# Optimization experiments

Hardware: AMD Instinct MI355X
Metric: run time of the kernel (lower is better)

## Reference

```python
import jax, jax.numpy as jnp
import numpy as np

N = 100000      # nodes
E = 1000000     # edges
D_IN = 64       # in_channels
HID = 64        # hid_channels
ENC = 64        # encoding_dim
OUT = 2         # out_channels (classes)
EDGE_DIM = 32   # TimeEncode dim == edge_dim
HEADS = 2
HD = HID // 2   # per-head channels (32)


def _p(k, shape):
    s = 1.0 / np.sqrt(shape[0])
    return jax.random.uniform(k, shape, jnp.float32, -s, s)


def setup_inputs() -> dict:
    key = jax.random.key(0)
    ks = jax.random.split(key, 40)
    inp = {
        "x": jax.random.normal(ks[0], (N, D_IN), jnp.float32),
        "edge_index": jax.random.randint(ks[1], (2, E), 0, N),
        "node_time": jax.random.uniform(ks[2], (N,), jnp.float32) * 100.0,
        "edge_time": jax.random.uniform(ks[3], (E, 1), jnp.float32) * 100.0,
        "node_mean_out_time_interval": jax.random.uniform(ks[4], (N,), jnp.float32) * 10.0,
        "node_out_degree": jax.random.uniform(ks[5], (N,), jnp.float32) * 50.0,
        "y": jax.random.randint(ks[6], (N,), 0, OUT),
        "train_mask": jnp.ones((N,), bool),
        # TimeEncode: cos(t W + b)
        "time_w": _p(ks[7], (1, EDGE_DIM)), "time_b": jnp.zeros((EDGE_DIM,), jnp.float32),
        # TemporalFrequencyEncoder / DegreeEncoder: Linear(1, ENC)
        "tf_w": _p(ks[8], (1, ENC)), "tf_b": jnp.zeros((ENC,), jnp.float32),
        "deg_w": _p(ks[9], (1, ENC)), "deg_b": jnp.zeros((ENC,), jnp.float32),
        # lin: Linear(in, hid)
        "lin_w": _p(ks[10], (D_IN, HID)), "lin_b": jnp.zeros((HID,), jnp.float32),
        # TransformerConv projections (heads*HD = HID)
        "Wq": _p(ks[11], (HID, HEADS * HD)), "bq": jnp.zeros((HEADS * HD,), jnp.float32),
        "Wk": _p(ks[12], (HID, HEADS * HD)), "bk": jnp.zeros((HEADS * HD,), jnp.float32),
        "Wv": _p(ks[13], (HID, HEADS * HD)), "bv": jnp.zeros((HEADS * HD,), jnp.float32),
        "We": _p(ks[14], (EDGE_DIM, HEADS * HD)), "be": jnp.zeros((HEADS * HD,), jnp.float32),
        "Wskip": _p(ks[15], (HID, HEADS * HD)), "bskip": jnp.zeros((HEADS * HD,), jnp.float32),
        # size-2 context attention
        "wenc_w": _p(ks[16], (ENC, ENC)), "wenc_b": jnp.zeros((ENC,), jnp.float32),
        "wx_w": _p(ks[17], (HID, ENC)), "wx_b": jnp.zeros((ENC,), jnp.float32),
        # lin_combine: Linear(hid+enc, hid)
        "comb_w": _p(ks[18], (HID + ENC, HID)), "comb_b": jnp.zeros((HID,), jnp.float32),
        # out: Linear(hid, out)
        "out_w": _p(ks[19], (HID, OUT)), "out_b": jnp.zeros((OUT,), jnp.float32),
    }
    return inp


def reference(x, edge_index, node_time, edge_time, node_mean_out_time_interval,
              node_out_degree, y, train_mask,
              time_w, time_b, tf_w, tf_b, deg_w, deg_b, lin_w, lin_b,
              Wq, bq, Wk, bk, Wv, bv, We, be, Wskip, bskip,
              wenc_w, wenc_b, wx_w, wx_b, comb_w, comb_b, out_w, out_b):
    src, dst = edge_index[0], edge_index[1]

    # relative edge time -> TimeEncode (cos features), used as edge_attr [E, 32]
    rel_t = node_time[src][:, None] - edge_time          # [E,1]
    rel_t_enc = jnp.cos(rel_t @ time_w + time_b)         # [E,EDGE_DIM]

    h = jax.nn.relu(x @ lin_w + lin_b)                   # [N,HID] (dropout = identity, eval)

    # TransformerConv (PyG math): per-edge attention + scatter-softmax aggregate
    q = (h @ Wq + bq).reshape(N, HEADS, HD)[dst]          # [E,H,HD]
    e = (rel_t_enc @ We + be).reshape(E, HEADS, HD)       # [E,H,HD]
    k = (h @ Wk + bk).reshape(N, HEADS, HD)[src] + e
    v = (h @ Wv + bv).reshape(N, HEADS, HD)[src] + e
    alpha = (q * k).sum(-1) / np.float32(np.sqrt(HD))     # [E,H]
    m = jax.ops.segment_max(alpha, dst, num_segments=N)   # stable softmax per dst node
    ea = jnp.exp(alpha - m[dst])
    denom = jax.ops.segment_sum(ea, dst, num_segments=N)
    a = ea / (denom[dst] + 1e-16)
    agg = jax.ops.segment_sum(a[:, :, None] * v, dst, num_segments=N)
    h1 = agg.reshape(N, HEADS * HD) + h @ Wskip + bskip   # concat heads + root skip

    # size-2 context attention over (temporal-frequency, degree) encodings
    tf_enc = node_mean_out_time_interval[:, None] @ tf_w + tf_b   # [N,ENC]
    deg_enc = node_out_degree[:, None] @ deg_w + deg_b            # [N,ENC]
    enc = jnp.stack((tf_enc, deg_enc), axis=1)                    # [N,2,ENC]
    enc_proj = jnp.tanh(enc @ wenc_w + wenc_b)                    # [N,2,ENC]
    x_proj = jnp.tanh(h1 @ wx_w + wx_b)                           # [N,ENC]
    score = jax.nn.softmax(jnp.einsum('nkd,nd->nk', enc_proj, x_proj), axis=1)  # [N,2]
    context = enc[:, 0] * score[:, 0:1] + enc[:, 1] * score[:, 1:2]

    h1 = jnp.concatenate((h1, context), axis=1) @ comb_w + comb_b  # [N,HID]
    logp = jax.nn.log_softmax(h1 @ out_w + out_b, axis=1)          # [N,OUT]
    return (h1, logp, y, train_mask)
```

## Files before the change

kernel.cpp:

```cpp
#include <hip/hip_runtime.h>
#include <hip/hip_fp16.h>

#define DEV __device__ __forceinline__

typedef _Float16 f16x8 __attribute__((ext_vector_type(8)));
typedef float f32x4 __attribute__((ext_vector_type(4)));

DEV float mask_val(const unsigned char* mb, int n) {
  unsigned b0 = mb[0], b1 = mb[1], b2 = mb[2], b3 = mb[3];
  if (b0 <= 1u && b1 == b0 && b2 == b0 && b3 == b0) {
    return mb[n] ? 1.f : 0.f;
  } else if (b1 == 0u && b2 == 0u && b3 == 0u) {
    return ((const int*)mb)[n] ? 1.f : 0.f;
  } else {
    return (((const float*)mb)[n] != 0.f) ? 1.f : 0.f;
  }
}

DEV float head_sum32(float x) {
  x += __int_as_float(__builtin_amdgcn_ds_swizzle(__float_as_int(x), 0x041F));
  x += __int_as_float(__builtin_amdgcn_ds_swizzle(__float_as_int(x), 0x081F));
  x += __int_as_float(__builtin_amdgcn_ds_swizzle(__float_as_int(x), 0x101F));
  x += __int_as_float(__builtin_amdgcn_ds_swizzle(__float_as_int(x), 0x201F));
  x += __int_as_float(__builtin_amdgcn_ds_swizzle(__float_as_int(x), 0x401F));
  return x;
}

__global__ void k_precompute(const float* __restrict__ tf_w, const float* __restrict__ tf_b,
                             const float* __restrict__ deg_w, const float* __restrict__ deg_b,
                             const float* __restrict__ wenc_w, const float* __restrict__ wenc_b,
                             const float* __restrict__ comb_w, float* __restrict__ cbuf) {
  int c = threadIdx.x;
  float A0 = 0, B0 = 0, A1 = 0, B1 = 0, P0 = 0, Q0 = 0, P1 = 0, Q1 = 0;
  for (int j = 0; j < 64; ++j) {
    float w  = wenc_w[j * 64 + c];
    float cw = comb_w[(64 + j) * 64 + c];
    float twj = tf_w[j], tbj = tf_b[j], dwj = deg_w[j], dbj = deg_b[j];
    A0 += twj * w;  B0 += tbj * w;
    A1 += dwj * w;  B1 += dbj * w;
    P0 += twj * cw; Q0 += tbj * cw;
    P1 += dwj * cw; Q1 += dbj * cw;
  }
  float wb = wenc_b[c];
  cbuf[c]       = A0; cbuf[64 + c]  = B0 + wb;
  cbuf[128 + c] = A1; cbuf[192 + c] = B1 + wb;
  cbuf[256 + c] = P0; cbuf[320 + c] = Q0;
  cbuf[384 + c] = P1; cbuf[448 + c] = Q1;
}

__global__ __launch_bounds__(256) void k_wcvt(
    const float* __restrict__ lin_w, const float* __restrict__ Wq,
    const float* __restrict__ Wk, const float* __restrict__ Wv,
    const float* __restrict__ Wsk, _Float16* __restrict__ wt) {
  const float* Ws[5] = {lin_w, Wq, Wk, Wv, Wsk};
  int idx = blockIdx.x * 256 + threadIdx.x;
  if (idx < 5 * 4096) {
    int s = idx >> 12, r = idx & 4095;
    int j = r >> 6, c = r & 63;
    wt[(s << 12) + c * 64 + j] = (_Float16)Ws[s][j * 64 + c];
  }
}

__global__ __launch_bounds__(256) void k_node_proj(
    const float* __restrict__ x, const _Float16* __restrict__ wt,
    const float* __restrict__ lin_b, const float* __restrict__ bq,
    const float* __restrict__ bk, const float* __restrict__ bv,
    const float* __restrict__ bsk, const float* __restrict__ be,
    float* __restrict__ q, __half2* __restrict__ kvp,
    float* __restrict__ skipout, int N) {
  __shared__ _Float16 H[4][16 * 72];
  const int tid = threadIdx.x;
  const int lane = tid & 63;
  const int wv = tid >> 6;
  const int mrow = lane & 15;
  const int kgrp = lane >> 4;
  const float invs = 0.17677669529663687f;
  float b_lin[4], b_q[4], b_k[4], b_v[4], b_sk[4];
#pragma unroll
  for (int nt = 0; nt < 4; ++nt) {
    const int cc = nt * 16 + mrow;
    b_lin[nt] = lin_b[cc];
    b_q[nt] = bq[cc];
    b_k[nt] = bk[cc] + be[cc];
    b_v[nt] = bv[cc] + be[cc];
    b_sk[nt] = bsk[cc];
  }
  _Float16* Hw = H[wv];
  const int ntiles = (N + 63) >> 6;
  for (int tile = blockIdx.x; tile < ntiles; tile += gridDim.x) {
    const int base = tile << 6;
    const int rowA = base + wv * 16 + mrow;
    const int rclamp = (rowA < N) ? rowA : (N - 1);
    const float* xr = x + (size_t)rclamp * 64 + kgrp * 8;
    const float4 u0 = *(const float4*)xr;
    const float4 u1 = *(const float4*)(xr + 4);
    const float4 u2 = *(const float4*)(xr + 32);
    const float4 u3 = *(const float4*)(xr + 36);
    const f16x8 a0 = {(_Float16)u0.x, (_Float16)u0.y, (_Float16)u0.z, (_Float16)u0.w,
                      (_Float16)u1.x, (_Float16)u1.y, (_Float16)u1.z, (_Float16)u1.w};
    const f16x8 a1 = {(_Float16)u2.x, (_Float16)u2.y, (_Float16)u2.z, (_Float16)u2.w,
                      (_Float16)u3.x, (_Float16)u3.y, (_Float16)u3.z, (_Float16)u3.w};
#pragma unroll
    for (int nt = 0; nt < 4; ++nt) {
      const _Float16* wb0 = wt + (nt * 16 + mrow) * 64 + kgrp * 8;
      const f16x8 B0 = *(const f16x8*)wb0;
      const f16x8 B1 = *(const f16x8*)(wb0 + 32);
      f32x4 C = {0.f, 0.f, 0.f, 0.f};
      C = __builtin_amdgcn_mfma_f32_16x16x32_f16(a0, B0, C, 0, 0, 0);
      C = __builtin_amdgcn_mfma_f32_16x16x32_f16(a1, B1, C, 0, 0, 0);
#pragma unroll
      for (int r = 0; r < 4; ++r) {
        const float hval = fmaxf(C[r] + b_lin[nt], 0.f);
        Hw[(kgrp * 4 + r) * 72 + nt * 16 + mrow] = (_Float16)hval;
      }
    }
    const f16x8 ha0 = *(const f16x8*)(Hw + mrow * 72 + kgrp * 8);
    const f16x8 ha1 = *(const f16x8*)(Hw + mrow * 72 + 32 + kgrp * 8);
    const int orow0 = base + wv * 16 + kgrp * 4;
#pragma unroll
    for (int nt = 0; nt < 4; ++nt) {
      const _Float16* wb0 = wt + 4096 + (nt * 16 + mrow) * 64 + kgrp * 8;
      const f16x8 B0 = *(const f16x8*)wb0;
      const f16x8 B1 = *(const f16x8*)(wb0 + 32);
      f32x4 C = {0.f, 0.f, 0.f, 0.f};
      C = __builtin_amdgcn_mfma_f32_16x16x32_f16(ha0, B0, C, 0, 0, 0);
      C = __builtin_amdgcn_mfma_f32_16x16x32_f16(ha1, B1, C, 0, 0, 0);
#pragma unroll
      for (int r = 0; r < 4; ++r) {
        const int orow = orow0 + r;
        if (orow < N) q[(size_t)orow * 64 + nt * 16 + mrow] = (C[r] + b_q[nt]) * invs;
      }
    }
#pragma unroll
    for (int nt = 0; nt < 4; ++nt) {
      const _Float16* wk0 = wt + 2 * 4096 + (nt * 16 + mrow) * 64 + kgrp * 8;
      const _Float16* wv0 = wt + 3 * 4096 + (nt * 16 + mrow) * 64 + kgrp * 8;
      const f16x8 Bk0 = *(const f16x8*)wk0;
      const f16x8 Bk1 = *(const f16x8*)(wk0 + 32);
      const f16x8 Bv0 = *(const f16x8*)wv0;
      const f16x8 Bv1 = *(const f16x8*)(wv0 + 32);
      f32x4 Ck = {0.f, 0.f, 0.f, 0.f};
      f32x4 Cv = {0.f, 0.f, 0.f, 0.f};
      Ck = __builtin_amdgcn_mfma_f32_16x16x32_f16(ha0, Bk0, Ck, 0, 0, 0);
      Ck = __builtin_amdgcn_mfma_f32_16x16x32_f16(ha1, Bk1, Ck, 0, 0, 0);
      Cv = __builtin_amdgcn_mfma_f32_16x16x32_f16(ha0, Bv0, Cv, 0, 0, 0);
      Cv = __builtin_amdgcn_mfma_f32_16x16x32_f16(ha1, Bv1, Cv, 0, 0, 0);
#pragma unroll
      for (int r = 0; r < 4; ++r) {
        const int orow = orow0 + r;
        if (orow < N)
          kvp[(size_t)orow * 64 + nt * 16 + mrow] =
              __halves2half2(__float2half_rn(Ck[r] + b_k[nt]), __float2half_rn(Cv[r] + b_v[nt]));
      }
    }
#pragma unroll
    for (int nt = 0; nt < 4; ++nt) {
      const _Float16* wb0 = wt + 4 * 4096 + (nt * 16 + mrow) * 64 + kgrp * 8;
      const f16x8 B0 = *(const f16x8*)wb0;
      const f16x8 B1 = *(const f16x8*)(wb0 + 32);
      f32x4 C = {0.f, 0.f, 0.f, 0.f};
      C = __builtin_amdgcn_mfma_f32_16x16x32_f16(ha0, B0, C, 0, 0, 0);
      C = __builtin_amdgcn_mfma_f32_16x16x32_f16(ha1, B1, C, 0, 0, 0);
#pragma unroll
      for (int r = 0; r < 4; ++r) {
        const int orow = orow0 + r;
        if (orow < N) skipout[(size_t)orow * 64 + nt * 16 + mrow] = C[r] + b_sk[nt];
      }
    }
  }
}

__global__ __launch_bounds__(256) void k_hist(const int* __restrict__ ei, int* __restrict__ counts, int E) {
  int i = blockIdx.x * 256 + threadIdx.x;
  if (i < E) atomicAdd(&counts[ei[E + i]], 1);
}

__global__ __launch_bounds__(256) void k_scan1(const int* __restrict__ counts, int* __restrict__ excl,
                                               int* __restrict__ bsum, int N) {
  __shared__ int s[256];
  const int t = threadIdx.x;
  const int idx = blockIdx.x * 256 + t;
  int val = (idx < N) ? counts[idx] : 0;
  s[t] = val;
  __syncthreads();
  for (int d = 1; d < 256; d <<= 1) {
    int add = (t >= d) ? s[t - d] : 0;
    __syncthreads();
    s[t] += add;
    __syncthreads();
  }
  if (idx < N) excl[idx] = s[t] - val;
  if (t == 255) bsum[blockIdx.x] = s[255];
}

__global__ __launch_bounds__(1024) void k_scan2(int* __restrict__ bsum, int B) {
  __shared__ int sm[1024];
  const int t = threadIdx.x;
  if (B <= 1024) {
    int val = (t < B) ? bsum[t] : 0;
    sm[t] = val;
    __syncthreads();
    for (int d = 1; d < 1024; d <<= 1) {
      int add = (t >= d) ? sm[t - d] : 0;
      __syncthreads();
      sm[t] += add;
      __syncthreads();
    }
    if (t < B) bsum[t] = sm[t] - val;
  } else if (t == 0) {
    int acc = 0;
    for (int i = 0; i < B; ++i) { int tt = bsum[i]; bsum[i] = acc; acc += tt; }
  }
}

__global__ __launch_bounds__(256) void k_scan3(const int* __restrict__ bsum, int* __restrict__ rowptr,
                                               int* __restrict__ next, int N, int E) {
  int i = blockIdx.x * 256 + threadIdx.x;
  if (i < N) {
    int r = rowptr[i] + bsum[i >> 8];
    rowptr[i] = r;
    next[i] = r;
  }
  if (i == 0) rowptr[N] = E;
}

__global__ __launch_bounds__(256) void k_fill(const int* __restrict__ ei,
                                              const float* __restrict__ node_time,
                                              const float* __restrict__ edge_time,
                                              int* __restrict__ next, int2* __restrict__ er, int E) {
  int e = blockIdx.x * 256 + threadIdx.x;
  if (e < E) {
    int s = ei[e], d = ei[E + e];
    int pos = atomicAdd(&next[d], 1);
    er[pos] = make_int2(s, __float_as_int(node_time[s] - edge_time[e]));
  }
}

__global__ __launch_bounds__(256) void k_aggregate(
    const int* __restrict__ rowptr, const int2* __restrict__ er,
    const float* __restrict__ q, const unsigned* __restrict__ kvu,
    const float* __restrict__ time_w, const float* __restrict__ time_b,
    const float* __restrict__ We,
    float* __restrict__ h1, int N) {
  __shared__ float swS[4][64];
  const int tid = threadIdx.x;
  const int c = tid & 63;
  const int wv = tid >> 6;
  const float INV2PI = 0.15915494309189535f;
  float wcol[32], Gw[32];
#pragma unroll
  for (int j = 0; j < 32; ++j) wcol[j] = We[j * 64 + c];
#pragma unroll
  for (int j = 0; j < 32; ++j) Gw[j] = We[(c & 31) * 64 + (c & 32) + j];
  const float tw = time_w[c & 31] * INV2PI;
  const float tb = time_b[c & 31] * INV2PI;
  const int h32 = c & 32;
  const int n0 = blockIdx.x * 4 + wv;
  const int nstride = gridDim.x * 4;
  for (int n = n0; n < N; n += nstride) {
    const int start = rowptr[n];
    const int end = rowptr[n + 1];
    const float qc = q[(size_t)n * 64 + c];
    swS[wv][c] = qc;
    float Gc = 0.f;
#pragma unroll
    for (int j = 0; j < 32; ++j) Gc = fmaf(swS[wv][h32 | j], Gw[j], Gc);
    float m = -1e30f, den = 0.f, num = 0.f, S = 0.f;
    for (int ce = start; ce < end; ce += 16) {
      const int cnt = (end - ce < 16) ? (end - ce) : 16;
      int src_[16];
      float rr_[16];
#pragma unroll
      for (int i = 0; i < 16; ++i) {
        const int ee = ce + ((i < cnt) ? i : cnt - 1);
        const int2 a = er[ee];
        src_[i] = a.x;
        rr_[i] = __int_as_float(a.y);
      }
      unsigned kvr[16];
#pragma unroll
      for (int i = 0; i < 16; ++i) kvr[i] = kvu[(size_t)src_[i] * 64 + c];
      float rv_[16], p[16];
#pragma unroll
      for (int i = 0; i < 16; ++i) {
        float ang = fmaf(rr_[i], tw, tb);
        ang = ang - floorf(ang);
        rv_[i] = __builtin_amdgcn_cosf(ang);
        const __half2 h2 = *(const __half2*)&kvr[i];
        p[i] = fmaf(rv_[i], Gc, qc * __half2float(h2.x));
      }
#pragma unroll
      for (int i = 0; i < 16; ++i) p[i] = head_sum32(p[i]);
#pragma unroll
      for (int i = 0; i < 16; ++i)
        if (i >= cnt) p[i] = -1e30f;
      float cm = p[0];
#pragma unroll
      for (int i = 1; i < 16; ++i) cm = fmaxf(cm, p[i]);
      const float mn = fmaxf(m, cm);
      const float sc = __expf(m - mn);
      num *= sc; den *= sc; S *= sc; m = mn;
#pragma unroll
      for (int i = 0; i < 16; ++i) {
        if (i < cnt) {
          const float ea = __expf(p[i] - m);
          const __half2 h2 = *(const __half2*)&kvr[i];
          num = fmaf(ea, __half2float(h2.y), num);
          S = fmaf(ea, rv_[i], S);
          den += ea;
        }
      }
    }
    swS[wv][c] = S;
    float econ = 0.f;
#pragma unroll
    for (int j = 0; j < 32; ++j) econ = fmaf(swS[wv][h32 | j], wcol[j], econ);
    const float agg = (num + econ) / (den + 1e-16f);
    h1[(size_t)n * 64 + c] = agg + h1[(size_t)n * 64 + c];
  }
}

__global__ __launch_bounds__(256) void k_epilogue(
    const float* __restrict__ t_int, const float* __restrict__ deg,
    const float* __restrict__ cbuf,
    const float* __restrict__ wx_w, const float* __restrict__ wx_b,
    const float* __restrict__ comb_w, const float* __restrict__ comb_b,
    const float* __restrict__ out_w, const float* __restrict__ out_b,
    const int* __restrict__ y, const unsigned char* __restrict__ maskb,
    float* __restrict__ out, int N) {
  __shared__ float sh[4][64];
  const int tid = threadIdx.x;
  const int c = tid & 63;
  const int wv = tid >> 6;
  float wxreg[64], cbreg[64];
#pragma unroll
  for (int j = 0; j < 64; ++j) { wxreg[j] = wx_w[j * 64 + c]; cbreg[j] = comb_w[j * 64 + c]; }
  const float A0 = cbuf[c], B0 = cbuf[64 + c], A1 = cbuf[128 + c], B1 = cbuf[192 + c];
  const float P0 = cbuf[256 + c], Q0 = cbuf[320 + c], P1 = cbuf[384 + c], Q1 = cbuf[448 + c];
  const float wxb = wx_b[c], cbb = comb_b[c];
  const float ow0 = out_w[c * 2 + 0], ow1 = out_w[c * 2 + 1];
  const float ob0 = out_b[0], ob1 = out_b[1];
  const size_t O1 = (size_t)N * 64;
  const size_t O2 = O1 + (size_t)N * 2;
  const size_t O3 = O2 + (size_t)N;
  const int ngroups = (N + 3) >> 2;
  for (int g = blockIdx.x; g < ngroups; g += gridDim.x) {
    const int n = g * 4 + wv;
    const bool act = n < N;
    float h1a = 0.f, ti = 0.f, dg = 0.f;
    if (act) {
      h1a = out[(size_t)n * 64 + c];
      ti = t_int[n];
      dg = deg[n];
    }
    sh[wv][c] = h1a;
    __syncthreads();
    const float4* hr = (const float4*)&sh[wv][0];
    float xp = wxb;
    float acc = cbb;
#pragma unroll
    for (int j4 = 0; j4 < 16; ++j4) {
      float4 hv = hr[j4];
      xp  = fmaf(hv.x, wxreg[4 * j4 + 0], xp);
      xp  = fmaf(hv.y, wxreg[4 * j4 + 1], xp);
      xp  = fmaf(hv.z, wxreg[4 * j4 + 2], xp);
      xp  = fmaf(hv.w, wxreg[4 * j4 + 3], xp);
      acc = fmaf(hv.x, cbreg[4 * j4 + 0], acc);
      acc = fmaf(hv.y, cbreg[4 * j4 + 1], acc);
      acc = fmaf(hv.z, cbreg[4 * j4 + 2], acc);
      acc = fmaf(hv.w, cbreg[4 * j4 + 3], acc);
    }
    xp = tanhf(xp);
    const float ep0 = tanhf(fmaf(ti, A0, B0));
    const float ep1 = tanhf(fmaf(dg, A1, B1));
    float d0 = ep0 * xp, d1 = ep1 * xp;
#pragma unroll
    for (int msk = 32; msk >= 1; msk >>= 1) { d0 += __shfl_xor(d0, msk, 64); d1 += __shfl_xor(d1, msk, 64); }
    const float mx = fmaxf(d0, d1);
    const float e0 = expf(d0 - mx), e1 = expf(d1 - mx);
    const float sden = e0 + e1;
    const float s0 = e0 / sden, s1 = e1 / sden;
    acc = fmaf(s0, fmaf(ti, P0, Q0), acc);
    acc = fmaf(s1, fmaf(dg, P1, Q1), acc);
    float z0 = acc * ow0, z1 = acc * ow1;
#pragma unroll
    for (int msk = 32; msk >= 1; msk >>= 1) { z0 += __shfl_xor(z0, msk, 64); z1 += __shfl_xor(z1, msk, 64); }
    if (act) {
      out[(size_t)n * 64 + c] = acc;
      if (c == 0) {
        z0 += ob0; z1 += ob1;
        const float mz = fmaxf(z0, z1);
        const float lse = mz + logf(expf(z0 - mz) + expf(z1 - mz));
        out[O1 + (size_t)n * 2 + 0] = z0 - lse;
        out[O1 + (size_t)n * 2 + 1] = z1 - lse;
        out[O2 + (size_t)n] = (float)y[n];
        out[O3 + (size_t)n] = mask_val(maskb, n);
      }
    }
    __syncthreads();
  }
}

extern "C" void kernel_launch(void* const* d_in, const int* in_sizes, int n_in,
                              void* d_out, int out_size, void* d_ws, size_t ws_size,
                              hipStream_t stream) {
  const float* x          = (const float*)d_in[0];
  const int*   ei         = (const int*)d_in[1];
  const float* node_time  = (const float*)d_in[2];
  const float* edge_time  = (const float*)d_in[3];
  const float* nmoti      = (const float*)d_in[4];
  const float* nod        = (const float*)d_in[5];
  const int*   y          = (const int*)d_in[6];
  const unsigned char* mask = (const unsigned char*)d_in[7];
  const float* time_w = (const float*)d_in[8];
  const float* time_b = (const float*)d_in[9];
  const float* tf_w   = (const float*)d_in[10];
  const float* tf_b   = (const float*)d_in[11];
  const float* deg_w  = (const float*)d_in[12];
  const float* deg_b  = (const float*)d_in[13];
  const float* lin_w  = (const float*)d_in[14];
  const float* lin_b  = (const float*)d_in[15];
  const float* Wq     = (const float*)d_in[16];
  const float* bq     = (const float*)d_in[17];
  const float* Wk     = (const float*)d_in[18];
  const float* bk     = (const float*)d_in[19];
  const float* Wv     = (const float*)d_in[20];
  const float* bv     = (const float*)d_in[21];
  const float* We     = (const float*)d_in[22];
  const float* be     = (const float*)d_in[23];
  const float* Wsk    = (const float*)d_in[24];
  const float* bsk    = (const float*)d_in[25];
  const float* wenc_w = (const float*)d_in[26];
  const float* wenc_b = (const float*)d_in[27];
  const float* wx_w   = (const float*)d_in[28];
  const float* wx_b   = (const float*)d_in[29];
  const float* comb_w = (const float*)d_in[30];
  const float* comb_b = (const float*)d_in[31];
  const float* out_w  = (const float*)d_in[32];
  const float* out_b  = (const float*)d_in[33];

  const int N = in_sizes[2];
  const int E = in_sizes[3];
  const size_t N64 = (size_t)N * 64;

  float*    q    = (float*)d_ws;
  __half2*  kvp  = (__half2*)(q + N64);
  int2*     er   = (int2*)((char*)kvp + N64 * sizeof(__half2));
  int*      counts = (int*)(er + E);
  int*      rowptr = counts + N;
  int*      next   = rowptr + N + 1;
  int*      bsum   = next + N;
  float*    cbuf   = (float*)(bsum + 4096);
  _Float16* wt     = (_Float16*)(cbuf + 512);
  float*    outf   = (float*)d_out;
  float*    skip   = outf;

  const int B = (N + 255) / 256;

  hipMemsetAsync(counts, 0, (size_t)N * sizeof(int), stream);

  k_precompute<<<1, 64, 0, stream>>>(tf_w, tf_b, deg_w, deg_b, wenc_w, wenc_b, comb_w, cbuf);
  k_wcvt<<<80, 256, 0, stream>>>(lin_w, Wq, Wk, Wv, Wsk, wt);

  const int ntiles = (N + 63) >> 6;
  k_node_proj<<<ntiles, 256, 0, stream>>>(x, wt, lin_b, bq, bk, bv, bsk, be,
                                          q, kvp, skip, N);

  const int EB = (E + 255) / 256;
  k_hist<<<EB, 256, 0, stream>>>(ei, counts, E);
  k_scan1<<<B, 256, 0, stream>>>(counts, rowptr, bsum, N);
  k_scan2<<<1, 1024, 0, stream>>>(bsum, B);
  k_scan3<<<B, 256, 0, stream>>>(bsum, rowptr, next, N, E);
  k_fill<<<EB, 256, 0, stream>>>(ei, node_time, edge_time, next, er, E);

  int agb = 768;
  if (agb > (N + 3) / 4) agb = (N + 3) / 4;
  k_aggregate<<<agb, 256, 0, stream>>>(rowptr, er, q, (const unsigned*)kvp,
                                       time_w, time_b, We, outf, N);

  k_epilogue<<<2048, 256, 0, stream>>>(nmoti, nod, cbuf, wx_w, wx_b,
                                       comb_w, comb_b, out_w, out_b, y, mask, outf, N);
}
```

Before: 414.1 us.

## Distribute softmax exps across lanes via LDS, merge setup kernels, drop barriers

In aggregation, each edge's exp weight is computed once by one lane and shared via LDS instead of every lane recomputing all 16 exps; row bounds are made scalar, the gather uses 32-bit indexing, and the skip value is loaded early. The two tiny setup kernels are fused into one launch, epilogue block barriers are removed since each wave uses its own shared slice, and the aggregate grid is enlarged. This relies on intra-wave LDS ordering without explicit barriers.

```diff
diff --git a/kernel.cpp b/kernel.cpp
--- a/kernel.cpp
+++ b/kernel.cpp
@@ -26,38 +26,40 @@
   return x;
 }
 
-__global__ void k_precompute(const float* __restrict__ tf_w, const float* __restrict__ tf_b,
-                             const float* __restrict__ deg_w, const float* __restrict__ deg_b,
-                             const float* __restrict__ wenc_w, const float* __restrict__ wenc_b,
-                             const float* __restrict__ comb_w, float* __restrict__ cbuf) {
-  int c = threadIdx.x;
-  float A0 = 0, B0 = 0, A1 = 0, B1 = 0, P0 = 0, Q0 = 0, P1 = 0, Q1 = 0;
-  for (int j = 0; j < 64; ++j) {
-    float w  = wenc_w[j * 64 + c];
-    float cw = comb_w[(64 + j) * 64 + c];
-    float twj = tf_w[j], tbj = tf_b[j], dwj = deg_w[j], dbj = deg_b[j];
-    A0 += twj * w;  B0 += tbj * w;
-    A1 += dwj * w;  B1 += dbj * w;
-    P0 += twj * cw; Q0 += tbj * cw;
-    P1 += dwj * cw; Q1 += dbj * cw;
-  }
-  float wb = wenc_b[c];
-  cbuf[c]       = A0; cbuf[64 + c]  = B0 + wb;
-  cbuf[128 + c] = A1; cbuf[192 + c] = B1 + wb;
-  cbuf[256 + c] = P0; cbuf[320 + c] = Q0;
-  cbuf[384 + c] = P1; cbuf[448 + c] = Q1;
-}
-
-__global__ __launch_bounds__(256) void k_wcvt(
+__global__ __launch_bounds__(256) void k_setup(
+    const float* __restrict__ tf_w, const float* __restrict__ tf_b,
+    const float* __restrict__ deg_w, const float* __restrict__ deg_b,
+    const float* __restrict__ wenc_w, const float* __restrict__ wenc_b,
+    const float* __restrict__ comb_w,
     const float* __restrict__ lin_w, const float* __restrict__ Wq,
     const float* __restrict__ Wk, const float* __restrict__ Wv,
-    const float* __restrict__ Wsk, _Float16* __restrict__ wt) {
-  const float* Ws[5] = {lin_w, Wq, Wk, Wv, Wsk};
-  int idx = blockIdx.x * 256 + threadIdx.x;
-  if (idx < 5 * 4096) {
-    int s = idx >> 12, r = idx & 4095;
-    int j = r >> 6, c = r & 63;
-    wt[(s << 12) + c * 64 + j] = (_Float16)Ws[s][j * 64 + c];
+    const float* __restrict__ Wsk,
+    float* __restrict__ cbuf, _Float16* __restrict__ wt) {
+  if (blockIdx.x < 80) {
+    const float* Ws[5] = {lin_w, Wq, Wk, Wv, Wsk};
+    int idx = blockIdx.x * 256 + threadIdx.x;
+    if (idx < 5 * 4096) {
+      int s = idx >> 12, r = idx & 4095;
+      int j = r >> 6, c = r & 63;
+      wt[(s << 12) + c * 64 + j] = (_Float16)Ws[s][j * 64 + c];
+    }
+  } else if (threadIdx.x < 64) {
+    int c = threadIdx.x;
+    float A0 = 0, B0 = 0, A1 = 0, B1 = 0, P0 = 0, Q0 = 0, P1 = 0, Q1 = 0;
+    for (int j = 0; j < 64; ++j) {
+      float w  = wenc_w[j * 64 + c];
+      float cw = comb_w[(64 + j) * 64 + c];
+      float twj = tf_w[j], tbj = tf_b[j], dwj = deg_w[j], dbj = deg_b[j];
+      A0 += twj * w;  B0 += tbj * w;
+      A1 += dwj * w;  B1 += dbj * w;
+      P0 += twj * cw; Q0 += tbj * cw;
+      P1 += dwj * cw; Q1 += dbj * cw;
+    }
+    float wb = wenc_b[c];
+    cbuf[c]       = A0; cbuf[64 + c]  = B0 + wb;
+    cbuf[128 + c] = A1; cbuf[192 + c] = B1 + wb;
+    cbuf[256 + c] = P0; cbuf[320 + c] = Q0;
+    cbuf[384 + c] = P1; cbuf[448 + c] = Q1;
   }
 }
 
@@ -243,6 +245,7 @@
     const float* __restrict__ We,
     float* __restrict__ h1, int N) {
   __shared__ float swS[4][64];
+  __shared__ float EAs[4][2][16];
   const int tid = threadIdx.x;
   const int c = tid & 63;
   const int wv = tid >> 6;
@@ -255,11 +258,15 @@
   const float tw = time_w[c & 31] * INV2PI;
   const float tb = time_b[c & 31] * INV2PI;
   const int h32 = c & 32;
+  const int lc = c & 15;
+  const bool writer = (c & 16) == 0;
+  float (*eaF)[16] = EAs[wv];
   const int n0 = blockIdx.x * 4 + wv;
   const int nstride = gridDim.x * 4;
   for (int n = n0; n < N; n += nstride) {
-    const int start = rowptr[n];
-    const int end = rowptr[n + 1];
+    const int start = __builtin_amdgcn_readfirstlane(rowptr[n]);
+    const int end = __builtin_amdgcn_readfirstlane(rowptr[n + 1]);
+    const float skipv = h1[(size_t)n * 64 + c];
     const float qc = q[(size_t)n * 64 + c];
     swS[wv][c] = qc;
     float Gc = 0.f;
@@ -279,7 +286,7 @@
       }
       unsigned kvr[16];
 #pragma unroll
-      for (int i = 0; i < 16; ++i) kvr[i] = kvu[(size_t)src_[i] * 64 + c];
+      for (int i = 0; i < 16; ++i) kvr[i] = kvu[(unsigned)(src_[i] * 64 + c)];
       float rv_[16], p[16];
 #pragma unroll
       for (int i = 0; i < 16; ++i) {
@@ -300,15 +307,26 @@
       const float mn = fmaxf(m, cm);
       const float sc = __expf(m - mn);
       num *= sc; den *= sc; S *= sc; m = mn;
+      if (writer) {
+        float pv = p[0];
+#pragma unroll
+        for (int i = 1; i < 16; ++i) pv = (lc == i) ? p[i] : pv;
+        eaF[c >> 5][lc] = __expf(pv - m);
+      }
+      const float* eah = eaF[h32 ? 1 : 0];
+      const float4 e0 = ((const float4*)eah)[0];
+      const float4 e1 = ((const float4*)eah)[1];
+      const float4 e2 = ((const float4*)eah)[2];
+      const float4 e3 = ((const float4*)eah)[3];
+      const float ea_[16] = {e0.x, e0.y, e0.z, e0.w, e1.x, e1.y, e1.z, e1.w,
+                             e2.x, e2.y, e2.z, e2.w, e3.x, e3.y, e3.z, e3.w};
 #pragma unroll
       for (int i = 0; i < 16; ++i) {
-        if (i < cnt) {
-          const float ea = __expf(p[i] - m);
-          const __half2 h2 = *(const __half2*)&kvr[i];
-          num = fmaf(ea, __half2float(h2.y), num);
-          S = fmaf(ea, rv_[i], S);
-          den += ea;
-        }
+        const float eai = ea_[i];
+        const __half2 h2 = *(const __half2*)&kvr[i];
+        num = fmaf(eai, __half2float(h2.y), num);
+        S = fmaf(eai, rv_[i], S);
+        den += eai;
       }
     }
     swS[wv][c] = S;
@@ -316,7 +334,7 @@
 #pragma unroll
     for (int j = 0; j < 32; ++j) econ = fmaf(swS[wv][h32 | j], wcol[j], econ);
     const float agg = (num + econ) / (den + 1e-16f);
-    h1[(size_t)n * 64 + c] = agg + h1[(size_t)n * 64 + c];
+    h1[(size_t)n * 64 + c] = agg + skipv;
   }
 }
 
@@ -354,7 +372,6 @@
       dg = deg[n];
     }
     sh[wv][c] = h1a;
-    __syncthreads();
     const float4* hr = (const float4*)&sh[wv][0];
     float xp = wxb;
     float acc = cbb;
@@ -397,7 +414,6 @@
         out[O3 + (size_t)n] = mask_val(maskb, n);
       }
     }
-    __syncthreads();
   }
 }
 
@@ -459,8 +475,8 @@
 
   hipMemsetAsync(counts, 0, (size_t)N * sizeof(int), stream);
 
-  k_precompute<<<1, 64, 0, stream>>>(tf_w, tf_b, deg_w, deg_b, wenc_w, wenc_b, comb_w, cbuf);
-  k_wcvt<<<80, 256, 0, stream>>>(lin_w, Wq, Wk, Wv, Wsk, wt);
+  k_setup<<<81, 256, 0, stream>>>(tf_w, tf_b, deg_w, deg_b, wenc_w, wenc_b, comb_w,
+                                  lin_w, Wq, Wk, Wv, Wsk, cbuf, wt);
 
   const int ntiles = (N + 63) >> 6;
   k_node_proj<<<ntiles, 256, 0, stream>>>(x, wt, lin_b, bq, bk, bv, bsk, be,
@@ -473,7 +489,7 @@
   k_scan3<<<B, 256, 0, stream>>>(bsum, rowptr, next, N, E);
   k_fill<<<EB, 256, 0, stream>>>(ei, node_time, edge_time, next, er, E);
 
-  int agb = 768;
+  int agb = 1024;
   if (agb > (N + 3) / 4) agb = (N + 3) / 4;
   k_aggregate<<<agb, 256, 0, stream>>>(rowptr, er, q, (const unsigned*)kvp,
                                        time_w, time_b, We, outf, N);
```

After: 410.9 us. About the same (-0.8%).
